# Optimization experiments

Measured on AMD Instinct MI355X. Metric: run time of the kernel, lower is better.

The kernel has to match this reference:

```python
import jax, jax.numpy as jnp
from jax import lax
import numpy as np

CHANNEL_N = 16
HIDDEN = 128
INPUT_CH = 1
KSIZE = 7
STEPS = 10
EPS = 1e-5


def setup_inputs() -> dict:
    key = jax.random.key(0)
    ks = jax.random.split(key, 8)
    B, H, W = 8, 256, 256
    x = jax.random.normal(ks[0], (B, H, W, CHANNEL_N), dtype=jnp.float32)
    # stochastic fire masks, one per step (torch: bernoulli_(p=fire_rate) under no_grad)
    masks = jax.random.bernoulli(ks[1], 0.5, (STEPS, B, 1, H, W))
    # depthwise conv: groups=channel_n -> weight [C,1,K,K]
    conv_w = jax.random.normal(ks[2], (CHANNEL_N, 1, KSIZE, KSIZE), dtype=jnp.float32) * 0.05
    conv_b = jax.random.normal(ks[3], (CHANNEL_N,), dtype=jnp.float32) * 0.05
    # fc0: 1x1 conv [hidden, 2*C]
    fc0_w = jax.random.normal(ks[4], (HIDDEN, 2 * CHANNEL_N), dtype=jnp.float32) * 0.1
    fc0_b = jax.random.normal(ks[5], (HIDDEN,), dtype=jnp.float32) * 0.05
    # fc1: 1x1 conv [C - input_channels, hidden], no bias (zero-init in torch; random here)
    fc1_w = jax.random.normal(ks[6], (CHANNEL_N - INPUT_CH, HIDDEN), dtype=jnp.float32) * 0.02
    bn_gamma = jnp.ones((HIDDEN,), dtype=jnp.float32)
    bn_beta = jnp.zeros((HIDDEN,), dtype=jnp.float32)
    return {"x": x, "masks": masks, "conv_w": conv_w, "conv_b": conv_b,
            "fc0_w": fc0_w, "fc0_b": fc0_b, "fc1_w": fc1_w,
            "bn_gamma": bn_gamma, "bn_beta": bn_beta}


def _nca_forward(x, masks, conv_w, conv_b, fc0_w, fc0_b, fc1_w, bn_gamma, bn_beta):
    state = jnp.transpose(x, (0, 3, 1, 2))  # b h w c -> b c h w
    const_in = state[:, :INPUT_CH]
    pad = (KSIZE - 1) // 2

    def step(state, mask):
        # depthwise 7x7 conv, reflect padding
        sp = jnp.pad(state, ((0, 0), (0, 0), (pad, pad), (pad, pad)), mode='reflect')
        d = lax.conv_general_dilated(
            sp, conv_w, window_strides=(1, 1), padding='VALID',
            dimension_numbers=('NCHW', 'OIHW', 'NCHW'),
            feature_group_count=CHANNEL_N)
        d = d + conv_b[None, :, None, None]
        cat = jnp.concatenate([state, d], axis=1)  # [B, 2C, H, W]
        # fc0 (1x1 conv)
        h = jnp.einsum('bchw,oc->bohw', cat, fc0_w) + fc0_b[None, :, None, None]
        # BatchNorm2d with batch statistics (track_running_stats=False)
        mean = jnp.mean(h, axis=(0, 2, 3), keepdims=True)
        var = jnp.var(h, axis=(0, 2, 3), keepdims=True)
        h = (h - mean) * lax.rsqrt(var + EPS)
        h = h * bn_gamma[None, :, None, None] + bn_beta[None, :, None, None]
        h = jax.nn.relu(h)
        # fc1 (1x1 conv, no bias)
        delta = jnp.einsum('bohw,ko->bkhw', h, fc1_w)  # [B, C-1, H, W]
        delta = delta * mask  # stochastic fire (broadcast over channels)
        new = state[:, INPUT_CH:] + delta
        return jnp.concatenate([const_in, new], axis=1), None

    state, _ = lax.scan(step, state, masks.astype(state.dtype))
    return jnp.transpose(state, (0, 2, 3, 1))  # b c h w -> b h w c


def reference(x, masks, conv_w, conv_b, fc0_w, fc0_b, fc1_w, bn_gamma, bn_beta):
    return _nca_forward(x, masks, conv_w, conv_b, fc0_w, fc0_b, fc1_w, bn_gamma, bn_beta)
```

## Files before the change

kernel.cpp:

```cpp
#include <hip/hip_runtime.h>

#define CH 16
#define HID 128
#define NB 8
#define NH 256
#define NW 256
#define NPX (NB*NH*NW)
#define NSTEP 10
#define GPW 8
#define KPW 2
#define SLAB 1280
#define NPART 64
#define PSTR 1088
#define POFF (NPART*PSTR)
#define STEPSTATS (POFF + 704)
#define SBLK 1024

typedef __attribute__((ext_vector_type(8))) short short8v;
typedef __attribute__((ext_vector_type(4))) float f32x4;

__device__ __forceinline__ int refl(int i, int n){
    if (i < 0) i = -i;
    if (i >= n) i = 2*n - 2 - i;
    return i;
}

__device__ __forceinline__ unsigned short f2bf(float x){
    unsigned int u = __float_as_uint(x);
    u += 0x7FFFu + ((u >> 16) & 1u);
    return (unsigned short)(u >> 16);
}
__device__ __forceinline__ float bf2f(unsigned short h){
    return __uint_as_float(((unsigned int)h) << 16);
}
__device__ __forceinline__ unsigned int cvtpk(float lo, float hi){
    unsigned int r;
    asm("v_cvt_pk_bf16_f32 %0, %1, %2" : "=v"(r) : "v"(lo), "v"(hi));
    return r;
}

__global__ void k_repack(const float* __restrict__ cw, const float* __restrict__ w0,
                         float* __restrict__ wp,
                         unsigned short* __restrict__ b0h, unsigned short* __restrict__ b0l){
    int t = blockIdx.x*256 + threadIdx.x;
    if (t < 49*16){ int tap = t >> 4, c = t & 15; wp[tap*16 + c] = cw[c*49 + tap]; }
    if (t < 4096){
        int n = t >> 9, l = (t >> 3) & 63, i = t & 7;
        int o = 16*n + (l & 15), k = ((l >> 4) << 3) + i;
        float v = w0[o*32 + k];
        unsigned short hi = f2bf(v);
        b0h[t] = hi;
        b0l[t] = f2bf(v - bf2f(hi));
    }
}

__global__ void k_zero(float* __restrict__ p, int n){
    int t = blockIdx.x*256 + threadIdx.x;
    if (t < n) p[t] = 0.f;
}

struct Row { float4 e[4]; float4 o[4]; };

__device__ __forceinline__ void fma4(float4& a, float4 w, float4 v){
    a.x += w.x*v.x; a.y += w.y*v.y; a.z += w.z*v.z; a.w += w.w*v.w;
}
__device__ __forceinline__ void ldrow(Row& r, const float4* L, int row, int tx){
    #pragma unroll
    for (int k=0;k<4;++k){
        r.e[k] = L[(row*2+0)*20 + tx + k];
        r.o[k] = L[(row*2+1)*20 + tx + k];
    }
}

__global__ __launch_bounds__(256,3)
void k_conv(const float* __restrict__ st, const float* __restrict__ wp,
            const float* __restrict__ cb, float* __restrict__ dout){
    __shared__ float4 tile4[38*2*20];
    __shared__ float4 cw4s[49];
    const int b = blockIdx.z >> 2, cg = blockIdx.z & 3;
    const int y0 = blockIdx.y*32, x0 = blockIdx.x*32;
    const int t = threadIdx.x;
    const int tx = t & 15, ty = t >> 4;

    if (t < 49) cw4s[t] = *(const float4*)&wp[t*16 + cg*4];
    for (int i = t; i < 38*38; i += 256){
        int py = i / 38, px = i - py*38;
        int gy = refl(y0 + py - 3, NH);
        int gx = refl(x0 + px - 3, NW);
        float4 v = *(const float4*)&st[(((size_t)b*NH + gy)*NW + gx)*CH + cg*4];
        tile4[(py*2 + (px&1))*20 + (px>>1)] = v;
    }
    __syncthreads();

    const float4* L = tile4;
    float4 bias = *(const float4*)&cb[cg*4];
    float4 a00 = bias, a01 = bias, a10 = bias, a11 = bias;
    Row A, B;
    ldrow(A, L, 2*ty,   tx);
    ldrow(B, L, 2*ty+1, tx);

#define CSTEP(dy, RA, RB, LOADNEXT, NR) \
    { \
        _Pragma("unroll") \
        for (int dx = 0; dx < 7; ++dx){ \
            float4 w4 = cw4s[(dy)*7 + dx]; \
            float4 v00 = ((dx)&1)   ? RA.o[(dx)>>1]   : RA.e[(dx)>>1]; \
            float4 v01 = ((dx+1)&1) ? RA.o[(dx+1)>>1] : RA.e[(dx+1)>>1]; \
            float4 v10 = ((dx)&1)   ? RB.o[(dx)>>1]   : RB.e[(dx)>>1]; \
            float4 v11 = ((dx+1)&1) ? RB.o[(dx+1)>>1] : RB.e[(dx+1)>>1]; \
            fma4(a00,w4,v00); fma4(a01,w4,v01); fma4(a10,w4,v10); fma4(a11,w4,v11); \
        } \
        if (LOADNEXT) ldrow(RA, L, NR, tx); \
    }

    CSTEP(0, A, B, 1, 2*ty+2)
    CSTEP(1, B, A, 1, 2*ty+3)
    CSTEP(2, A, B, 1, 2*ty+4)
    CSTEP(3, B, A, 1, 2*ty+5)
    CSTEP(4, A, B, 1, 2*ty+6)
    CSTEP(5, B, A, 1, 2*ty+7)
    CSTEP(6, A, B, 0, 0)
#undef CSTEP

    const size_t pr = ((size_t)b*NH + (size_t)(y0 + 2*ty))*NW + (x0 + 2*tx);
    *(float4*)&dout[(pr)*CH + cg*4]        = a00;
    *(float4*)&dout[(pr+1)*CH + cg*4]      = a01;
    *(float4*)&dout[(pr+NW)*CH + cg*4]     = a10;
    *(float4*)&dout[(pr+NW+1)*CH + cg*4]   = a11;
}

__global__ __launch_bounds__(512)
void k_stats(const float* __restrict__ st, const float* __restrict__ dv,
             float* __restrict__ S,
             const float* __restrict__ w0g, const float* __restrict__ b0,
             const float* __restrict__ gam, const float* __restrict__ bet,
             const float* __restrict__ f1){
    __shared__ float lds[8*SLAB];
    __shared__ int isLast;
    const int t = threadIdx.x, lane = t & 63, w = t >> 6;
    const int lo = lane & 15, hi = lane >> 4;
    float* slab = &lds[w*SLAB];
    const int gw = blockIdx.x*8 + w;

    short8v ones;
    {
        short ov = (lo == 0) ? (short)0x3F80 : (short)0;
        #pragma unroll
        for (int i=0;i<8;++i) ones[i] = ov;
    }
    f32x4 a00 = (f32x4){0.f,0.f,0.f,0.f};
    f32x4 a01 = a00, a11 = a00, s0 = a00, s1 = a00;

    const int lp = lane >> 3, lq = lane & 7;
    const float* lbase = (lq < 4) ? st : dv;
    const int lch = (lq & 3) * 4;
    const size_t p0 = (size_t)gw * (KPW*32);

    float4 v[KPW][4];
    #pragma unroll
    for (int j=0;j<KPW;++j)
        #pragma unroll
        for (int j2=0;j2<4;++j2)
            v[j][j2] = *(const float4*)&lbase[(p0 + j*32 + lp + 8*j2)*CH + lch];

    #pragma unroll
    for (int j=0;j<KPW;++j){
        #pragma unroll
        for (int j2=0;j2<4;++j2){
            int p = lp + 8*j2;
            *(float2*)&slab[p*34 + lq*4]     = make_float2(v[j][j2].x, v[j][j2].y);
            *(float2*)&slab[p*34 + lq*4 + 2] = make_float2(v[j][j2].z, v[j][j2].w);
        }
        short8v r0h, r0l, r1h, r1l;
        #pragma unroll
        for (int ct=0;ct<2;++ct){
            #pragma unroll
            for (int i=0;i<8;++i){
                float f = slab[(hi*8+i)*34 + ct*16 + lo];
                unsigned int u = __float_as_uint(f);
                unsigned short ah = (unsigned short)(u >> 16);
                float r = f - __uint_as_float(u & 0xFFFF0000u);
                unsigned short al = (unsigned short)(__float_as_uint(r) >> 16);
                if (ct==0){ r0h[i]=(short)ah; r0l[i]=(short)al; }
                else      { r1h[i]=(short)ah; r1l[i]=(short)al; }
            }
        }
        s0 = __builtin_amdgcn_mfma_f32_16x16x32_bf16(ones, r0h, s0, 0,0,0);
        s0 = __builtin_amdgcn_mfma_f32_16x16x32_bf16(ones, r0l, s0, 0,0,0);
        s1 = __builtin_amdgcn_mfma_f32_16x16x32_bf16(ones, r1h, s1, 0,0,0);
        s1 = __builtin_amdgcn_mfma_f32_16x16x32_bf16(ones, r1l, s1, 0,0,0);
        a00 = __builtin_amdgcn_mfma_f32_16x16x32_bf16(r0h, r0h, a00, 0,0,0);
        a00 = __builtin_amdgcn_mfma_f32_16x16x32_bf16(r0l, r0h, a00, 0,0,0);
        a00 = __builtin_amdgcn_mfma_f32_16x16x32_bf16(r0h, r0l, a00, 0,0,0);
        a11 = __builtin_amdgcn_mfma_f32_16x16x32_bf16(r1h, r1h, a11, 0,0,0);
        a11 = __builtin_amdgcn_mfma_f32_16x16x32_bf16(r1l, r1h, a11, 0,0,0);
        a11 = __builtin_amdgcn_mfma_f32_16x16x32_bf16(r1h, r1l, a11, 0,0,0);
        a01 = __builtin_amdgcn_mfma_f32_16x16x32_bf16(r0h, r1h, a01, 0,0,0);
        a01 = __builtin_amdgcn_mfma_f32_16x16x32_bf16(r0l, r1h, a01, 0,0,0);
        a01 = __builtin_amdgcn_mfma_f32_16x16x32_bf16(r0h, r1l, a01, 0,0,0);
    }

    float* red = lds;
    #pragma unroll
    for (int k=0;k<4;++k){
        red[t*20 + k]      = a00[k];
        red[t*20 + 4 + k]  = a01[k];
        red[t*20 + 8 + k]  = a11[k];
        red[t*20 + 12 + k] = s0[k];
        red[t*20 + 16 + k] = s1[k];
    }
    __syncthreads();
    if (w == 0){
        float tmp[20];
        #pragma unroll
        for (int k=0;k<20;++k){
            float s = 0.f;
            #pragma unroll
            for (int ww=0;ww<8;++ww) s += red[(lane + 64*ww)*20 + k];
            tmp[k] = s;
        }
        float* part = S + (size_t)(blockIdx.x & (NPART-1))*PSTR;
        #pragma unroll
        for (int r=0;r<4;++r){
            atomicAdd(&part[(hi*4+r)*32 + lo],        tmp[r]);
            atomicAdd(&part[(hi*4+r)*32 + 16 + lo],   tmp[4+r]);
            atomicAdd(&part[(16+hi*4+r)*32 + 16+lo],  tmp[8+r]);
        }
        if (hi == 0){
            atomicAdd(&part[1024 + lo],      tmp[12]);
            atomicAdd(&part[1024 + 16 + lo], tmp[16]);
        }
        __threadfence();
        if (lane == 0){
            unsigned int* ctr = (unsigned int*)(S + POFF + 640);
            unsigned int prev = atomicAdd(ctr, 1u);
            isLast = (prev == SBLK - 1);
        }
    }
    __syncthreads();
    if (!isLast) return;
    __threadfence();

    for (int e = t; e < 1056; e += 512){
        float s = 0.f;
        #pragma unroll 4
        for (int p = 0; p < NPART; ++p) s += S[(size_t)p*PSTR + e];
        lds[e] = s;
    }
    __syncthreads();
    if (t < 128){
        const int o = t;
        const float inv = 1.f / (float)NPX;
        float wv[32];
        #pragma unroll
        for (int c=0;c<32;++c) wv[c] = w0g[o*32+c];
        float m1 = 0.f;
        #pragma unroll
        for (int c=0;c<32;++c) m1 += wv[c]*lds[1024+c];
        m1 *= inv;
        float q = 0.f;
        #pragma unroll
        for (int i=0;i<32;++i){
            float ti = 0.f;
            #pragma unroll
            for (int j=0;j<32;++j){
                float sv = (i >= 16 && j < 16) ? lds[j*32+i] : lds[i*32+j];
                ti += sv*wv[j];
            }
            q += wv[i]*ti;
        }
        q *= inv;
        float var = q - m1*m1;
        float rstd = rsqrtf(var + 1e-5f);
        float mean = m1 + b0[o];
        float scale = rstd * gam[o];
        S[POFF + o] = bet[o]/scale + b0[o] - mean;
        unsigned short* f1sh = (unsigned short*)(S + POFF + 128);
        const int base = (o>>5)*512 + ((o>>3)&3)*128 + (o&7);
        f1sh[base] = 0;
        #pragma unroll
        for (int c=1;c<16;++c)
            f1sh[base + c*8] = f2bf(f1[(c-1)*HID + o] * scale);
    }
}

__global__ __launch_bounds__(256)
void k_update(const float* __restrict__ st, const float* __restrict__ dv,
              const int* __restrict__ msk,
              const unsigned short* __restrict__ gb0h, const unsigned short* __restrict__ gb0l,
              const float* __restrict__ Sstep, float* __restrict__ out){
    __shared__ __align__(16) unsigned int hls[4*16*68];
    const int lane = threadIdx.x & 63, w = threadIdx.x >> 6;
    const int lo16 = lane & 15, qw = lane >> 4;
    unsigned int* hb = &hls[w*16*68];

    const short8v* p0h = (const short8v*)gb0h;
    const short8v* p0l = (const short8v*)gb0l;
    const short8v* p1h = (const short8v*)(Sstep + POFF + 128);
    short8v B0h[8], B0l[8], B1h[4];
    #pragma unroll
    for (int n=0;n<8;++n){ B0h[n] = p0h[n*64 + lane]; B0l[n] = p0l[n*64 + lane]; }
    #pragma unroll
    for (int tt=0;tt<4;++tt) B1h[tt] = p1h[tt*64 + lane];
    const float* shb = Sstep + POFF;
    float4 shbv[8];
    #pragma unroll
    for (int n=0;n<8;++n) shbv[n] = *(const float4*)&shb[16*n + 4*qw];

    const int gw = blockIdx.x*4 + w;
    const float* abase = (qw < 2) ? st : dv;
    const int choff = (qw & 1)*8;

    for (int gi = 0; gi < GPW; ++gi){
        const size_t pg0 = ((size_t)gw*GPW + gi)*16;
        const float* ap = abase + (pg0 + lo16)*CH + choff;
        float4 v0 = *(const float4*)ap;
        float4 v1 = *(const float4*)(ap + 4);
        float av[8] = {v0.x,v0.y,v0.z,v0.w,v1.x,v1.y,v1.z,v1.w};
        short8v ah, al;
        #pragma unroll
        for (int i=0;i<8;++i){
            unsigned int u = __float_as_uint(av[i]);
            ah[i] = (short)(unsigned short)(u >> 16);
            float r = av[i] - __uint_as_float(u & 0xFFFF0000u);
            al[i] = (short)(unsigned short)(__float_as_uint(r) >> 16);
        }
        f32x4 acc[8];
        #pragma unroll
        for (int n=0;n<8;++n)
            acc[n] = (f32x4){shbv[n].x, shbv[n].y, shbv[n].z, shbv[n].w};
        #pragma unroll
        for (int n=0;n<8;++n){
            acc[n] = __builtin_amdgcn_mfma_f32_16x16x32_bf16(B0h[n], ah, acc[n], 0,0,0);
            acc[n] = __builtin_amdgcn_mfma_f32_16x16x32_bf16(B0h[n], al, acc[n], 0,0,0);
            acc[n] = __builtin_amdgcn_mfma_f32_16x16x32_bf16(B0l[n], ah, acc[n], 0,0,0);
        }
        #pragma unroll
        for (int n=0;n<8;++n){
            float h0 = fmaxf(acc[n][0], 0.f), h1 = fmaxf(acc[n][1], 0.f);
            float h2 = fmaxf(acc[n][2], 0.f), h3 = fmaxf(acc[n][3], 0.f);
            unsigned int wa = cvtpk(h0, h1), wb = cvtpk(h2, h3);
            *(uint2*)&hb[lo16*68 + 8*n + 2*qw] = make_uint2(wa, wb);
        }
        f32x4 dacc = (f32x4){0.f,0.f,0.f,0.f};
        #pragma unroll
        for (int tt=0;tt<4;++tt){
            short8v ah2 = *(const short8v*)&hb[lo16*68 + 16*tt + 4*qw];
            dacc = __builtin_amdgcn_mfma_f32_16x16x32_bf16(B1h[tt], ah2, dacc, 0,0,0);
        }
        const size_t p = pg0 + lo16;
        float4 stv = *(const float4*)&st[p*CH + 4*qw];
        const float m = (float)msk[p];
        float4 ov;
        ov.x = stv.x + dacc[0]*m;
        ov.y = stv.y + dacc[1]*m;
        ov.z = stv.z + dacc[2]*m;
        ov.w = stv.w + dacc[3]*m;
        *(float4*)&out[p*CH + 4*qw] = ov;
    }
}

extern "C" void kernel_launch(void* const* d_in, const int* in_sizes, int n_in,
                              void* d_out, int out_size, void* d_ws, size_t ws_size,
                              hipStream_t stream){
    const float* x   = (const float*)d_in[0];
    const int*   mk  = (const int*)d_in[1];
    const float* cw  = (const float*)d_in[2];
    const float* cb  = (const float*)d_in[3];
    const float* w0  = (const float*)d_in[4];
    const float* b0  = (const float*)d_in[5];
    const float* f1  = (const float*)d_in[6];
    const float* gam = (const float*)d_in[7];
    const float* bet = (const float*)d_in[8];

    float* ws    = (float*)d_ws;
    float* dbuf  = ws;
    float* sbuf  = ws + (size_t)NPX*CH;
    float* stats = ws + (size_t)2*NPX*CH;
    float* wp    = stats + (size_t)NSTEP*STEPSTATS;
    unsigned short* b0h = (unsigned short*)(wp + 800);
    unsigned short* b0l = b0h + 4096;

    k_repack<<<16,256,0,stream>>>(cw, w0, wp, b0h, b0l);
    k_zero<<<(NSTEP*STEPSTATS+255)/256,256,0,stream>>>(stats, NSTEP*STEPSTATS);

    const float* cur = x;
    float* outp = (float*)d_out;
    for (int s=0;s<NSTEP;++s){
        float* S = stats + (size_t)s*STEPSTATS;
        float* nxt = (s & 1) ? outp : sbuf;
        k_conv<<<dim3(NW/32,NH/32,NB*4),256,0,stream>>>(cur, wp, cb, dbuf);
        k_stats<<<SBLK,512,0,stream>>>(cur, dbuf, S, w0, b0, gam, bet, f1);
        k_update<<<NPX/16/4/GPW,256,0,stream>>>(cur, dbuf, mk + (size_t)s*NPX,
                                                b0h, b0l, S, nxt);
        cur = nxt;
    }
}
```

Measured before the change: 1.142 ms.

## Fuse all NCA steps into one persistent cooperative kernel with grid syncs

Replaces the per-step launches of the conv, stats and update kernels with a single cooperative persistent kernel. Blocks loop over conv tiles, stats chunks and update chunks, and grid-wide barriers separate the phases. BN finalization runs on block 0 between two barriers. This removes about thirty kernel launches and the last-block atomic counter, but adds four grid syncs per step, a serialized single-block finalize phase, and a grid capped at 1024 blocks. A fallback multi-kernel path remains for when the cooperative launch fails.

```diff
diff --git a/kernel.cpp b/kernel.cpp
--- a/kernel.cpp
+++ b/kernel.cpp
@@ -1,4 +1,7 @@
 #include <hip/hip_runtime.h>
+#include <hip/hip_cooperative_groups.h>
+
+namespace cg = cooperative_groups;
 
 #define CH 16
 #define HID 128
@@ -10,11 +13,11 @@
 #define GPW 8
 #define KPW 2
 #define SLAB 1280
-#define NPART 64
+#define NPART 32
 #define PSTR 1088
-#define POFF (NPART*PSTR)
-#define STEPSTATS (POFF + 704)
-#define SBLK 1024
+#define PART_END (NPART*PSTR)
+#define STEPSTATS (PART_END + 128 + 1024)
+#define MAXGRID 1024
 
 typedef __attribute__((ext_vector_type(8))) short short8v;
 typedef __attribute__((ext_vector_type(4))) float f32x4;
@@ -24,7 +27,6 @@
     if (i >= n) i = 2*n - 2 - i;
     return i;
 }
-
 __device__ __forceinline__ unsigned short f2bf(float x){
     unsigned int u = __float_as_uint(x);
     u += 0x7FFFu + ((u >> 16) & 1u);
@@ -60,7 +62,6 @@
 }
 
 struct Row { float4 e[4]; float4 o[4]; };
-
 __device__ __forceinline__ void fma4(float4& a, float4 w, float4 v){
     a.x += w.x*v.x; a.y += w.y*v.y; a.z += w.z*v.z; a.w += w.w*v.w;
 }
@@ -72,33 +73,31 @@
     }
 }
 
-__global__ __launch_bounds__(256,3)
-void k_conv(const float* __restrict__ st, const float* __restrict__ wp,
-            const float* __restrict__ cb, float* __restrict__ dout){
-    __shared__ float4 tile4[38*2*20];
-    __shared__ float4 cw4s[49];
-    const int b = blockIdx.z >> 2, cg = blockIdx.z & 3;
-    const int y0 = blockIdx.y*32, x0 = blockIdx.x*32;
-    const int t = threadIdx.x;
-    const int tx = t & 15, ty = t >> 4;
-
-    if (t < 49) cw4s[t] = *(const float4*)&wp[t*16 + cg*4];
+
+__device__ __forceinline__ void conv_unit(int u, int t, const float* __restrict__ cur,
+                                          const float* __restrict__ wp, const float* __restrict__ cb,
+                                          float* __restrict__ dbuf, char* smem){
+    float4* tile4 = (float4*)smem;
+    float4* cw4s  = (float4*)(smem + 24320);
+    const int bz = u >> 6, b = bz >> 2, cgr = bz & 3;
+    const int yy0 = ((u >> 3) & 7)*32, xx0 = (u & 7)*32;
+    __syncthreads();
+    if (t < 49) cw4s[t] = *(const float4*)&wp[t*16 + cgr*4];
     for (int i = t; i < 38*38; i += 256){
         int py = i / 38, px = i - py*38;
-        int gy = refl(y0 + py - 3, NH);
-        int gx = refl(x0 + px - 3, NW);
-        float4 v = *(const float4*)&st[(((size_t)b*NH + gy)*NW + gx)*CH + cg*4];
+        int gy = refl(yy0 + py - 3, NH);
+        int gx = refl(xx0 + px - 3, NW);
+        float4 v = *(const float4*)&cur[(((size_t)b*NH + gy)*NW + gx)*CH + cgr*4];
         tile4[(py*2 + (px&1))*20 + (px>>1)] = v;
     }
     __syncthreads();
-
+    const int tx = t & 15, ty = t >> 4;
     const float4* L = tile4;
-    float4 bias = *(const float4*)&cb[cg*4];
+    float4 bias = *(const float4*)&cb[cgr*4];
     float4 a00 = bias, a01 = bias, a10 = bias, a11 = bias;
     Row A, B;
     ldrow(A, L, 2*ty,   tx);
     ldrow(B, L, 2*ty+1, tx);
-
 #define CSTEP(dy, RA, RB, LOADNEXT, NR) \
     { \
         _Pragma("unroll") \
@@ -112,7 +111,6 @@
         } \
         if (LOADNEXT) ldrow(RA, L, NR, tx); \
     }
-
     CSTEP(0, A, B, 1, 2*ty+2)
     CSTEP(1, B, A, 1, 2*ty+3)
     CSTEP(2, A, B, 1, 2*ty+4)
@@ -121,48 +119,27 @@
     CSTEP(5, B, A, 1, 2*ty+7)
     CSTEP(6, A, B, 0, 0)
 #undef CSTEP
-
-    const size_t pr = ((size_t)b*NH + (size_t)(y0 + 2*ty))*NW + (x0 + 2*tx);
-    *(float4*)&dout[(pr)*CH + cg*4]        = a00;
-    *(float4*)&dout[(pr+1)*CH + cg*4]      = a01;
-    *(float4*)&dout[(pr+NW)*CH + cg*4]     = a10;
-    *(float4*)&dout[(pr+NW+1)*CH + cg*4]   = a11;
-}
-
-__global__ __launch_bounds__(512)
-void k_stats(const float* __restrict__ st, const float* __restrict__ dv,
-             float* __restrict__ S,
-             const float* __restrict__ w0g, const float* __restrict__ b0,
-             const float* __restrict__ gam, const float* __restrict__ bet,
-             const float* __restrict__ f1){
-    __shared__ float lds[8*SLAB];
-    __shared__ int isLast;
-    const int t = threadIdx.x, lane = t & 63, w = t >> 6;
+    const size_t pr = ((size_t)b*NH + (size_t)(yy0 + 2*ty))*NW + (xx0 + 2*tx);
+    *(float4*)&dbuf[(pr)*CH + cgr*4]      = a00;
+    *(float4*)&dbuf[(pr+1)*CH + cgr*4]    = a01;
+    *(float4*)&dbuf[(pr+NW)*CH + cgr*4]   = a10;
+    *(float4*)&dbuf[(pr+NW+1)*CH + cgr*4] = a11;
+}
+
+__device__ __forceinline__ void stats_chunk(size_t p0, int lane,
+                                            const float* __restrict__ st, const float* __restrict__ dv,
+                                            float* slab, const short8v& ones,
+                                            f32x4& a00, f32x4& a01, f32x4& a11, f32x4& s0, f32x4& s1){
     const int lo = lane & 15, hi = lane >> 4;
-    float* slab = &lds[w*SLAB];
-    const int gw = blockIdx.x*8 + w;
-
-    short8v ones;
-    {
-        short ov = (lo == 0) ? (short)0x3F80 : (short)0;
-        #pragma unroll
-        for (int i=0;i<8;++i) ones[i] = ov;
-    }
-    f32x4 a00 = (f32x4){0.f,0.f,0.f,0.f};
-    f32x4 a01 = a00, a11 = a00, s0 = a00, s1 = a00;
-
     const int lp = lane >> 3, lq = lane & 7;
     const float* lbase = (lq < 4) ? st : dv;
     const int lch = (lq & 3) * 4;
-    const size_t p0 = (size_t)gw * (KPW*32);
-
     float4 v[KPW][4];
     #pragma unroll
     for (int j=0;j<KPW;++j)
         #pragma unroll
         for (int j2=0;j2<4;++j2)
             v[j][j2] = *(const float4*)&lbase[(p0 + j*32 + lp + 8*j2)*CH + lch];
-
     #pragma unroll
     for (int j=0;j<KPW;++j){
         #pragma unroll
@@ -199,8 +176,15 @@
         a01 = __builtin_amdgcn_mfma_f32_16x16x32_bf16(r0l, r1h, a01, 0,0,0);
         a01 = __builtin_amdgcn_mfma_f32_16x16x32_bf16(r0h, r1l, a01, 0,0,0);
     }
-
-    float* red = lds;
+}
+
+__device__ __forceinline__ void stats_epilogue(int t, int nwaves, float* red,
+                                               const f32x4& a00, const f32x4& a01, const f32x4& a11,
+                                               const f32x4& s0, const f32x4& s1,
+                                               float* __restrict__ part){
+    const int lane = t & 63, w = t >> 6;
+    const int lo = lane & 15, hi = lane >> 4;
+    (void)w;
     #pragma unroll
     for (int k=0;k<4;++k){
         red[t*20 + k]      = a00[k];
@@ -210,16 +194,14 @@
         red[t*20 + 16 + k] = s1[k];
     }
     __syncthreads();
-    if (w == 0){
+    if (t < 64){
         float tmp[20];
         #pragma unroll
         for (int k=0;k<20;++k){
-            float s = 0.f;
-            #pragma unroll
-            for (int ww=0;ww<8;++ww) s += red[(lane + 64*ww)*20 + k];
-            tmp[k] = s;
-        }
-        float* part = S + (size_t)(blockIdx.x & (NPART-1))*PSTR;
+            float sm = 0.f;
+            for (int ww=0;ww<nwaves;++ww) sm += red[(lane + 64*ww)*20 + k];
+            tmp[k] = sm;
+        }
         #pragma unroll
         for (int r=0;r<4;++r){
             atomicAdd(&part[(hi*4+r)*32 + lo],        tmp[r]);
@@ -230,22 +212,19 @@
             atomicAdd(&part[1024 + lo],      tmp[12]);
             atomicAdd(&part[1024 + 16 + lo], tmp[16]);
         }
-        __threadfence();
-        if (lane == 0){
-            unsigned int* ctr = (unsigned int*)(S + POFF + 640);
-            unsigned int prev = atomicAdd(ctr, 1u);
-            isLast = (prev == SBLK - 1);
-        }
-    }
-    __syncthreads();
-    if (!isLast) return;
-    __threadfence();
-
-    for (int e = t; e < 1056; e += 512){
-        float s = 0.f;
-        #pragma unroll 4
-        for (int p = 0; p < NPART; ++p) s += S[(size_t)p*PSTR + e];
-        lds[e] = s;
+    }
+}
+
+__device__ __forceinline__ void finalize_body(int t, int nthreads, float* lds,
+                                              const float* __restrict__ S,
+                                              const float* __restrict__ w0g, const float* __restrict__ b0v,
+                                              const float* __restrict__ gamv, const float* __restrict__ betv,
+                                              const float* __restrict__ f1v, float* __restrict__ Sout){
+    for (int e = t; e < 1056; e += nthreads){
+        float sm = 0.f;
+        #pragma unroll 8
+        for (int p = 0; p < NPART; ++p) sm += S[(size_t)p*PSTR + e];
+        lds[e] = sm;
     }
     __syncthreads();
     if (t < 128){
@@ -272,47 +251,29 @@
         q *= inv;
         float var = q - m1*m1;
         float rstd = rsqrtf(var + 1e-5f);
-        float mean = m1 + b0[o];
-        float scale = rstd * gam[o];
-        S[POFF + o] = bet[o]/scale + b0[o] - mean;
-        unsigned short* f1sh = (unsigned short*)(S + POFF + 128);
+        float mean = m1 + b0v[o];
+        float scale = rstd * gamv[o];
+        Sout[PART_END + o] = betv[o]/scale + b0v[o] - mean;
+        unsigned short* f1sh = (unsigned short*)(Sout + PART_END + 128);
         const int base = (o>>5)*512 + ((o>>3)&3)*128 + (o&7);
         f1sh[base] = 0;
         #pragma unroll
         for (int c=1;c<16;++c)
-            f1sh[base + c*8] = f2bf(f1[(c-1)*HID + o] * scale);
-    }
-}
-
-__global__ __launch_bounds__(256)
-void k_update(const float* __restrict__ st, const float* __restrict__ dv,
-              const int* __restrict__ msk,
-              const unsigned short* __restrict__ gb0h, const unsigned short* __restrict__ gb0l,
-              const float* __restrict__ Sstep, float* __restrict__ out){
-    __shared__ __align__(16) unsigned int hls[4*16*68];
-    const int lane = threadIdx.x & 63, w = threadIdx.x >> 6;
+            f1sh[base + c*8] = f2bf(f1v[(c-1)*HID + o] * scale);
+    }
+}
+
+__device__ __forceinline__ void update_wavechunk(int gwu, int lane, unsigned int* hb,
+                                                 const float* __restrict__ st, const float* __restrict__ dv,
+                                                 const int* __restrict__ msk,
+                                                 const short8v* B0h, const short8v* B0l, const short8v* B1h,
+                                                 const float4* shbv, float* __restrict__ out){
     const int lo16 = lane & 15, qw = lane >> 4;
-    unsigned int* hb = &hls[w*16*68];
-
-    const short8v* p0h = (const short8v*)gb0h;
-    const short8v* p0l = (const short8v*)gb0l;
-    const short8v* p1h = (const short8v*)(Sstep + POFF + 128);
-    short8v B0h[8], B0l[8], B1h[4];
-    #pragma unroll
-    for (int n=0;n<8;++n){ B0h[n] = p0h[n*64 + lane]; B0l[n] = p0l[n*64 + lane]; }
-    #pragma unroll
-    for (int tt=0;tt<4;++tt) B1h[tt] = p1h[tt*64 + lane];
-    const float* shb = Sstep + POFF;
-    float4 shbv[8];
-    #pragma unroll
-    for (int n=0;n<8;++n) shbv[n] = *(const float4*)&shb[16*n + 4*qw];
-
-    const int gw = blockIdx.x*4 + w;
     const float* abase = (qw < 2) ? st : dv;
     const int choff = (qw & 1)*8;
-
+    #pragma unroll 1
     for (int gi = 0; gi < GPW; ++gi){
-        const size_t pg0 = ((size_t)gw*GPW + gi)*16;
+        const size_t pg0 = ((size_t)gwu*GPW + gi)*16;
         const float* ap = abase + (pg0 + lo16)*CH + choff;
         float4 v0 = *(const float4*)ap;
         float4 v1 = *(const float4*)(ap + 4);
@@ -358,6 +319,145 @@
         ov.w = stv.w + dacc[3]*m;
         *(float4*)&out[p*CH + 4*qw] = ov;
     }
+}
+
+__global__ __launch_bounds__(256,4)
+void k_mega(const float* __restrict__ x, const int* __restrict__ mk,
+            float* __restrict__ dbuf, float* __restrict__ sbuf, float* __restrict__ outp,
+            float* __restrict__ stats, const float* __restrict__ wp,
+            const float* __restrict__ cb,
+            const unsigned short* __restrict__ gb0h, const unsigned short* __restrict__ gb0l,
+            const float* __restrict__ w0g, const float* __restrict__ b0v,
+            const float* __restrict__ gamv, const float* __restrict__ betv,
+            const float* __restrict__ f1v){
+    cg::grid_group gridg = cg::this_grid();
+    __shared__ __align__(16) char smem[25152];
+    const int t = threadIdx.x;
+    const int bid = blockIdx.x;
+    const int G = gridDim.x;
+    const int lane = t & 63, w = t >> 6;
+
+    const float* cur = x;
+    #pragma unroll 1
+    for (int s = 0; s < NSTEP; ++s){
+        float* nxt = (s & 1) ? outp : sbuf;
+        float* S = stats + (size_t)s*STEPSTATS;
+        const int* msk = mk + (size_t)s*NPX;
+
+        #pragma unroll 1
+        for (int u = bid; u < 2048; u += G)
+            conv_unit(u, t, cur, wp, cb, dbuf, smem);
+        gridg.sync();
+
+        {
+            float* lds = (float*)smem;
+            float* slab = &lds[w*SLAB];
+            short8v ones;
+            {
+                short ov = ((lane & 15) == 0) ? (short)0x3F80 : (short)0;
+                #pragma unroll
+                for (int i=0;i<8;++i) ones[i] = ov;
+            }
+            f32x4 a00 = (f32x4){0.f,0.f,0.f,0.f};
+            f32x4 a01 = a00, a11 = a00, s0 = a00, s1 = a00;
+            #pragma unroll 1
+            for (int gw = bid*4 + w; gw < 8192; gw += G*4)
+                stats_chunk((size_t)gw*(KPW*32), lane, cur, dbuf, slab, ones, a00, a01, a11, s0, s1);
+            __syncthreads();
+            stats_epilogue(t, 4, lds, a00, a01, a11, s0, s1,
+                           S + (size_t)(bid & (NPART-1))*PSTR);
+        }
+        gridg.sync();
+
+        if (bid == 0)
+            finalize_body(t, 256, (float*)smem, S, w0g, b0v, gamv, betv, f1v, S);
+        gridg.sync();
+
+        {
+            unsigned int* hls = (unsigned int*)smem;
+            unsigned int* hb = &hls[w*16*68];
+            const short8v* p0h = (const short8v*)gb0h;
+            const short8v* p0l = (const short8v*)gb0l;
+            const short8v* p1h = (const short8v*)(S + PART_END + 128);
+            short8v B0h[8], B0l[8], B1h[4];
+            #pragma unroll
+            for (int n=0;n<8;++n){ B0h[n] = p0h[n*64 + lane]; B0l[n] = p0l[n*64 + lane]; }
+            #pragma unroll
+            for (int tt=0;tt<4;++tt) B1h[tt] = p1h[tt*64 + lane];
+            const float* shb = S + PART_END;
+            const int qw = lane >> 4;
+            float4 shbv[8];
+            #pragma unroll
+            for (int n=0;n<8;++n) shbv[n] = *(const float4*)&shb[16*n + 4*qw];
+            __syncthreads();
+            #pragma unroll 1
+            for (int gwu = bid*4 + w; gwu < 4096; gwu += G*4)
+                update_wavechunk(gwu, lane, hb, cur, dbuf, msk, B0h, B0l, B1h, shbv, nxt);
+        }
+        gridg.sync();
+        cur = nxt;
+    }
+}
+
+__global__ __launch_bounds__(256,3)
+void k_conv_fb(const float* __restrict__ st, const float* __restrict__ wp,
+               const float* __restrict__ cb, float* __restrict__ dout){
+    __shared__ __align__(16) char smem[25104];
+    const int u = ((int)blockIdx.z << 6) | ((int)blockIdx.y << 3) | (int)blockIdx.x;
+    conv_unit(u, threadIdx.x, st, wp, cb, dout, smem);
+}
+
+__global__ __launch_bounds__(512)
+void k_stats_fb(const float* __restrict__ st, const float* __restrict__ dv,
+                float* __restrict__ S){
+    __shared__ float lds[8*SLAB];
+    const int t = threadIdx.x, lane = t & 63, w = t >> 6;
+    float* slab = &lds[w*SLAB];
+    const int gw = blockIdx.x*8 + w;
+    short8v ones;
+    {
+        short ov = ((lane & 15) == 0) ? (short)0x3F80 : (short)0;
+        #pragma unroll
+        for (int i=0;i<8;++i) ones[i] = ov;
+    }
+    f32x4 a00 = (f32x4){0.f,0.f,0.f,0.f};
+    f32x4 a01 = a00, a11 = a00, s0 = a00, s1 = a00;
+    stats_chunk((size_t)gw*(KPW*32), lane, st, dv, slab, ones, a00, a01, a11, s0, s1);
+    __syncthreads();
+    stats_epilogue(t, 8, lds, a00, a01, a11, s0, s1,
+                   S + (size_t)(blockIdx.x & (NPART-1))*PSTR);
+}
+
+__global__ void k_finalize_fb(const float* __restrict__ Sin,
+                              const float* __restrict__ w0g, const float* __restrict__ b0v,
+                              const float* __restrict__ gamv, const float* __restrict__ betv,
+                              const float* __restrict__ f1v, float* __restrict__ Sout){
+    __shared__ float Ssm[1056];
+    finalize_body(threadIdx.x, 512, Ssm, Sin, w0g, b0v, gamv, betv, f1v, Sout);
+}
+
+__global__ __launch_bounds__(256)
+void k_update_fb(const float* __restrict__ st, const float* __restrict__ dv,
+                 const int* __restrict__ msk,
+                 const unsigned short* __restrict__ gb0h, const unsigned short* __restrict__ gb0l,
+                 const float* __restrict__ Sstep, float* __restrict__ out){
+    __shared__ __align__(16) unsigned int hls[4*16*68];
+    const int lane = threadIdx.x & 63, w = threadIdx.x >> 6;
+    unsigned int* hb = &hls[w*16*68];
+    const short8v* p0h = (const short8v*)gb0h;
+    const short8v* p0l = (const short8v*)gb0l;
+    const short8v* p1h = (const short8v*)(Sstep + PART_END + 128);
+    short8v B0h[8], B0l[8], B1h[4];
+    #pragma unroll
+    for (int n=0;n<8;++n){ B0h[n] = p0h[n*64 + lane]; B0l[n] = p0l[n*64 + lane]; }
+    #pragma unroll
+    for (int tt=0;tt<4;++tt) B1h[tt] = p1h[tt*64 + lane];
+    const float* shb = Sstep + PART_END;
+    const int qw = lane >> 4;
+    float4 shbv[8];
+    #pragma unroll
+    for (int n=0;n<8;++n) shbv[n] = *(const float4*)&shb[16*n + 4*qw];
+    update_wavechunk(blockIdx.x*4 + w, lane, hb, st, dv, msk, B0h, B0l, B1h, shbv, out);
 }
 
 extern "C" void kernel_launch(void* const* d_in, const int* in_sizes, int n_in,
@@ -380,19 +480,41 @@
     float* wp    = stats + (size_t)NSTEP*STEPSTATS;
     unsigned short* b0h = (unsigned short*)(wp + 800);
     unsigned short* b0l = b0h + 4096;
+    float* outp = (float*)d_out;
 
     k_repack<<<16,256,0,stream>>>(cw, w0, wp, b0h, b0l);
     k_zero<<<(NSTEP*STEPSTATS+255)/256,256,0,stream>>>(stats, NSTEP*STEPSTATS);
 
-    const float* cur = x;
-    float* outp = (float*)d_out;
-    for (int s=0;s<NSTEP;++s){
-        float* S = stats + (size_t)s*STEPSTATS;
-        float* nxt = (s & 1) ? outp : sbuf;
-        k_conv<<<dim3(NW/32,NH/32,NB*4),256,0,stream>>>(cur, wp, cb, dbuf);
-        k_stats<<<SBLK,512,0,stream>>>(cur, dbuf, S, w0, b0, gam, bet, f1);
-        k_update<<<NPX/16/4/GPW,256,0,stream>>>(cur, dbuf, mk + (size_t)s*NPX,
-                                                b0h, b0l, S, nxt);
-        cur = nxt;
-    }
-}
+    int dev = 0;
+    (void)hipGetDevice(&dev);
+    int numCU = 0;
+    (void)hipDeviceGetAttribute(&numCU, hipDeviceAttributeMultiprocessorCount, dev);
+    int maxB = 0;
+    hipError_t orc = hipOccupancyMaxActiveBlocksPerMultiprocessor(&maxB, k_mega, 256, 0);
+    int G = (orc == hipSuccess && numCU > 0) ? maxB * numCU : 0;
+    if (G > MAXGRID) G = MAXGRID;
+
+    bool ran = false;
+    if (G >= 64){
+        void* args[] = { (void*)&x, (void*)&mk, (void*)&dbuf, (void*)&sbuf, (void*)&outp,
+                         (void*)&stats, (void*)&wp, (void*)&cb, (void*)&b0h, (void*)&b0l,
+                         (void*)&w0, (void*)&b0, (void*)&gam, (void*)&bet, (void*)&f1 };
+        hipError_t rc = hipLaunchCooperativeKernel(k_mega, dim3(G), dim3(256),
+                                                   args, 0u, stream);
+        ran = (rc == hipSuccess);
+    }
+
+    if (!ran){
+        const float* cur = x;
+        for (int s=0;s<NSTEP;++s){
+            float* S = stats + (size_t)s*STEPSTATS;
+            float* nxt = (s & 1) ? outp : sbuf;
+            k_conv_fb<<<dim3(8,8,32),256,0,stream>>>(cur, wp, cb, dbuf);
+            k_stats_fb<<<1024,512,0,stream>>>(cur, dbuf, S);
+            k_finalize_fb<<<1,512,0,stream>>>(S, w0, b0, gam, bet, f1, S);
+            k_update_fb<<<1024,256,0,stream>>>(cur, dbuf, mk + (size_t)s*NPX,
+                                               b0h, b0l, S, nxt);
+            cur = nxt;
+        }
+    }
+}
```

Measured after the change: 4.082 ms. 257% more time.
